# Optimization experiments

Measured on AMD Instinct MI355X. Metric: run time of the kernel, lower is better.

The kernel has to match this reference:

```python
import jax, jax.numpy as jnp
import numpy as np
import math

B, NO, ML, D, H = 32, 512, 512, 1024, 16


def setup_inputs() -> dict:
    key = jax.random.key(0)
    ks = jax.random.split(key, 16)
    v = jax.random.normal(ks[0], (B, NO, D), jnp.float32)
    t = jax.random.normal(ks[1], (B, ML, D), jnp.float32)
    # valid-length prefix masks (float, as in the torch module)
    v_len = jax.random.randint(ks[2], (B,), NO // 2, NO + 1)
    t_len = jax.random.randint(ks[3], (B,), ML // 2, ML + 1)
    v_mask = (jnp.arange(NO)[None, :] < v_len[:, None]).astype(jnp.float32)
    t_mask = (jnp.arange(ML)[None, :] < t_len[:, None]).astype(jnp.float32)
    lin = lambda k, din, dout: jax.random.normal(k, (din, dout), jnp.float32) * 0.02
    return {
        "v": v, "t": t, "v_mask": v_mask, "t_mask": t_mask,
        "W_v4t": lin(ks[4], D, D), "b_v4t": jnp.zeros((D,), jnp.float32),
        "W_t4v": lin(ks[5], D, D), "b_t4v": jnp.zeros((D,), jnp.float32),
        "W_v": lin(ks[6], D, 3 * D), "b_v": jnp.zeros((3 * D,), jnp.float32),
        "W_t": lin(ks[7], D, 3 * D), "b_t": jnp.zeros((3 * D,), jnp.float32),
        "W_vo": lin(ks[8], D, D), "b_vo": jnp.zeros((D,), jnp.float32),
        "W_to": lin(ks[9], D, D), "b_to": jnp.zeros((D,), jnp.float32),
        "num_head": H,
    }


def _heads(x, h, dh):
    b, n, _ = x.shape
    return x.reshape(b, n, h, dh).transpose(0, 2, 1, 3)  # [B,H,N,dh]


def _unheads(x):
    b, h, n, dh = x.shape
    return x.transpose(0, 2, 1, 3).reshape(b, n, h * dh)


def _attend(q, k, val, mask, gate, h, dh):
    # gate: [B, D] -> per-head diag scale [B,H,1,dh]
    g = 1.0 + gate.reshape(-1, h, 1, dh)
    scores = jnp.einsum('bhqd,bhkd->bhqk', g * q, g * k) / math.sqrt(dh)
    scores = jnp.where(mask[:, None, None, :] > 0, scores, -jnp.inf)
    attn = jax.nn.softmax(scores, axis=-1)
    return _unheads(jnp.einsum('bhqk,bhkd->bhqd', attn, val))


def reference(v, t, v_mask, t_mask, W_v4t, b_v4t, W_t4v, b_t4v,
              W_v, b_v, W_t, b_t, W_vo, b_vo, W_to, b_to, num_head):
    d = v.shape[-1]
    dh = d // num_head
    # masked mean pooling per modality
    v_mean = (v * v_mask[:, :, None]).sum(1) / v_mask.sum(1, keepdims=True)
    t_mean = (t * t_mask[:, :, None]).sum(1) / t_mask.sum(1, keepdims=True)
    v4t_gate = jax.nn.sigmoid(jax.nn.relu(v_mean) @ W_v4t + b_v4t)  # [B,D]
    t4v_gate = jax.nn.sigmoid(jax.nn.relu(t_mean) @ W_t4v + b_t4v)
    # fused KQV projections, masked
    v_trans = (jax.nn.relu(v) @ W_v + b_v) * v_mask[:, :, None]
    t_trans = (jax.nn.relu(t) @ W_t + b_t) * t_mask[:, :, None]
    # torch split order: k, q, v
    v_k, v_q, v_v = (_heads(v_trans[..., i * d:(i + 1) * d], num_head, dh) for i in range(3))
    t_k, t_q, t_v = (_heads(t_trans[..., i * d:(i + 1) * d], num_head, dh) for i in range(3))
    v_update = _attend(v_q, v_k, v_v, v_mask, t4v_gate, num_head, dh)
    t_update = _attend(t_q, t_k, t_v, t_mask, v4t_gate, num_head, dh)
    updated_v = (v + v_update) @ W_vo + b_vo
    updated_t = (t + t_update) @ W_to + b_to
    return updated_v, updated_t
```

## Files before the change

### kernel.cpp

```cpp
#include <hip/hip_runtime.h>
#include <hip/hip_bf16.h>
#include <math.h>

#define B_   32
#define NO_  512
#define D_   1024
#define H_   16
#define DH_  64
#define D3_  3072

typedef __hip_bfloat16 bf16;
typedef short short8  __attribute__((ext_vector_type(8)));
typedef short short4v __attribute__((ext_vector_type(4)));
typedef float f32x4   __attribute__((ext_vector_type(4)));

__device__ inline short f2bf(float x) {
  bf16 h = __float2bfloat16(x);
  return *reinterpret_cast<short*>(&h);
}
__device__ inline float bf2f(short s) {
  union { unsigned int u; float f; } cv;
  cv.u = ((unsigned int)(unsigned short)s) << 16;
  return cv.f;
}

__device__ inline void gload_lds16(const void* g, void* l) {
  __builtin_amdgcn_global_load_lds(
      (__attribute__((address_space(1))) void*)(void*)(g),
      (__attribute__((address_space(3))) void*)(l), 16, 0, 0);
}

__global__ __launch_bounds__(256) void pool_kernel(
    const float* __restrict__ v, const float* __restrict__ t,
    const float* __restrict__ vmask, const float* __restrict__ tmask,
    float* __restrict__ vmean, float* __restrict__ tmean) {
  const float* x; const float* m; float* out;
  if (blockIdx.y == 0) { x = v; m = vmask; out = vmean; }
  else                 { x = t; m = tmask; out = tmean; }
  int b = blockIdx.x >> 2;
  int d = ((blockIdx.x & 3) << 8) + threadIdx.x;
  float acc = 0.f, msum = 0.f;
  const float* xp = x + ((size_t)b * NO_) * D_ + d;
  const float* mp = m + b * NO_;
  for (int n = 0; n < NO_; ++n) {
    float mv = mp[n];
    acc  += xp[(size_t)n * D_] * mv;
    msum += mv;
  }
  out[b * D_ + d] = acc / msum;
}

__global__ __launch_bounds__(256) void gate_kernel(
    const float* __restrict__ vmean, const float* __restrict__ tmean,
    const float* __restrict__ Wv4t, const float* __restrict__ bv4t,
    const float* __restrict__ Wt4v, const float* __restrict__ bt4v,
    float* __restrict__ gv4t, float* __restrict__ gt4v) {
  const float* mean; const float* W; const float* bias; float* out;
  if (blockIdx.y == 0) { mean = vmean; W = Wv4t; bias = bv4t; out = gv4t; }
  else                 { mean = tmean; W = Wt4v; bias = bt4v; out = gt4v; }
  int b = blockIdx.x >> 2;
  int j = ((blockIdx.x & 3) << 8) + threadIdx.x;
  const float* mb = mean + b * D_;
  float acc = bias[j];
  for (int k = 0; k < D_; ++k) {
    float mv = mb[k]; mv = mv > 0.f ? mv : 0.f;
    acc += mv * W[(size_t)k * D_ + j];
  }
  out[b * D_ + j] = 1.f / (1.f + expf(-acc));
}

__global__ __launch_bounds__(256) void wtrans_kernel(
    const float* __restrict__ W, short* __restrict__ Wt, int K, int N) {
  __shared__ float tile[32][33];
  int n0 = blockIdx.x * 32, k0 = blockIdx.y * 32;
  int tx = threadIdx.x & 31, ty = threadIdx.x >> 5;
#pragma unroll
  for (int i = 0; i < 4; ++i) {
    int kk = ty + i * 8;
    tile[kk][tx] = W[(size_t)(k0 + kk) * N + n0 + tx];
  }
  __syncthreads();
#pragma unroll
  for (int i = 0; i < 4; ++i) {
    int nn = ty + i * 8;
    Wt[(size_t)(n0 + nn) * K + k0 + tx] = f2bf(tile[tx][nn]);
  }
}

__global__ __launch_bounds__(256) void reluconv_kernel(
    const float* __restrict__ x, short* __restrict__ y) {
  int i = (blockIdx.x * 256 + threadIdx.x) * 4;
  float4 vv = *(const float4*)(x + i);
  short4v o;
  o[0] = f2bf(vv.x > 0.f ? vv.x : 0.f);
  o[1] = f2bf(vv.y > 0.f ? vv.y : 0.f);
  o[2] = f2bf(vv.z > 0.f ? vv.z : 0.f);
  o[3] = f2bf(vv.w > 0.f ? vv.w : 0.f);
  *(short4v*)(y + i) = o;
}

__device__ __forceinline__ void stage_half(const short* __restrict__ g,
                                           short* l, int wave, int lane) {
#pragma unroll
  for (int r2 = 0; r2 < 2; ++r2) {
    int ob  = r2 * 8192 + wave * 1024;
    int o   = ob + lane * 16;
    int row = o >> 7;
    int kb  = (o & 127) ^ ((row & 7) << 4);
    gload_lds16(g + (size_t)row * D_ + (kb >> 1), l + (ob >> 1));
  }
}

__device__ __forceinline__ void read_a4(short8 (&a)[4][2], const short* As,
                                        int baseRow, int col, int qb) {
#pragma unroll
  for (int m = 0; m < 4; ++m) {
    int row = baseRow + m * 16 + col;
    int sw  = (row & 7) << 4;
    a[m][0] = *(const short8*)(As + (((row << 7) + (qb ^ sw)) >> 1));
    a[m][1] = *(const short8*)(As + (((row << 7) + ((64 + qb) ^ sw)) >> 1));
  }
}

__device__ __forceinline__ void read_b2(short8 (&b)[2][2], const short* Bs,
                                        int baseRow, int col, int qb) {
#pragma unroll
  for (int n = 0; n < 2; ++n) {
    int row = baseRow + n * 16 + col;
    int sw  = (row & 7) << 4;
    b[n][0] = *(const short8*)(Bs + (((row << 7) + (qb ^ sw)) >> 1));
    b[n][1] = *(const short8*)(Bs + (((row << 7) + ((64 + qb) ^ sw)) >> 1));
  }
}

template<int MH, int NH>
__device__ __forceinline__ void mma8(f32x4 (&acc)[8][4],
                                     const short8 (&a)[4][2],
                                     const short8 (&b)[2][2]) {
#pragma unroll
  for (int m = 0; m < 4; ++m)
#pragma unroll
    for (int n = 0; n < 2; ++n)
#pragma unroll
      for (int kh = 0; kh < 2; ++kh)
        acc[MH * 4 + m][NH * 2 + n] = __builtin_amdgcn_mfma_f32_16x16x32_bf16(
            a[m][kh], b[n][kh], acc[MH * 4 + m][NH * 2 + n], 0, 0, 0);
}

#define PHASE_TAIL(MH, NH, BR)                              \
  __builtin_amdgcn_s_barrier();                             \
  asm volatile("s_waitcnt lgkmcnt(0)" ::: "memory");        \
  __builtin_amdgcn_s_setprio(1);                            \
  mma8<MH, NH>(acc, a, BR);                                 \
  __builtin_amdgcn_s_setprio(0);                            \
  __builtin_amdgcn_s_barrier();

template<int SA, int SB, int VMN>
__device__ __forceinline__ void ktile(
    f32x4 (&acc)[8][4], short8 (&a)[4][2], short8 (&b0)[2][2], short8 (&b1)[2][2],
    const short* Asc, const short* Bsc, short* Asn, short* Bsn,
    const short* gA, const short* gB,
    int wm, int wn, int col, int qb, int wave, int lane) {
  read_a4(a, Asc, wm * 128, col, qb);
  read_b2(b0, Bsc, wn * 64, col, qb);
  if constexpr (SA) stage_half(gA, Asn, wave, lane);
  PHASE_TAIL(0, 0, b0)
  read_b2(b1, Bsc, wn * 64 + 32, col, qb);
  if constexpr (SA) stage_half(gA + 128 * D_, Asn + 8192, wave, lane);
  PHASE_TAIL(0, 1, b1)
  read_a4(a, Asc, wm * 128 + 64, col, qb);
  if constexpr (SB) stage_half(gB, Bsn, wave, lane);
  PHASE_TAIL(1, 0, b0)
  if constexpr (SB) stage_half(gB + 128 * D_, Bsn + 8192, wave, lane);
  __builtin_amdgcn_s_barrier();
  __builtin_amdgcn_s_setprio(1);
  mma8<1, 1>(acc, a, b1);
  __builtin_amdgcn_s_setprio(0);
  if constexpr (VMN >= 0)
    asm volatile("s_waitcnt vmcnt(%0)" :: "i"(VMN) : "memory");
  __builtin_amdgcn_s_barrier();
}

template<int EPI>
__global__ __launch_bounds__(512, 2) void mfma_gemm256_kernel(
    const short* __restrict__ A, const short* __restrict__ Bt,
    const float* __restrict__ bias, const float* __restrict__ mask,
    void* __restrict__ Cout, int M, int N) {
  __shared__ short lds[65536];
  short* As0 = lds;
  short* Bs0 = lds + 16384;
  short* As1 = lds + 32768;
  short* Bs1 = lds + 49152;

  const int tid  = threadIdx.x;
  const int wave = tid >> 6, lane = tid & 63;
  const int col  = lane & 15, quad = lane >> 4, qb = quad << 4;
  const int wm   = wave >> 2, wn = wave & 3;

  const int nx   = gridDim.x;
  const int orig = blockIdx.y * nx + blockIdx.x;
  const int cpx  = (nx * gridDim.y) >> 3;
  const int swz  = (orig & 7) * cpx + (orig >> 3);
  const int bx   = swz % nx;
  const int by   = swz / nx;
  const int rowBase = by * 256;
  const int colBase = bx * 256;

  const short* gA = A  + (size_t)rowBase * D_;
  const short* gB = Bt + (size_t)colBase * D_;

  f32x4 zero = {0.f, 0.f, 0.f, 0.f};
  f32x4 acc[8][4];
#pragma unroll
  for (int i = 0; i < 8; ++i)
#pragma unroll
    for (int j = 0; j < 4; ++j) acc[i][j] = zero;

  short8 a[4][2], b0[2][2], b1[2][2];

  stage_half(gA,                 As0,        wave, lane);
  stage_half(gA + 128 * D_,      As0 + 8192, wave, lane);
  stage_half(gB,                 Bs0,        wave, lane);
  stage_half(gB + 128 * D_,      Bs0 + 8192, wave, lane);
  stage_half(gB + 64,            Bs1,        wave, lane);
  stage_half(gB + 64 + 128 * D_, Bs1 + 8192, wave, lane);
  asm volatile("s_waitcnt vmcnt(4)" ::: "memory");
  __builtin_amdgcn_s_barrier();

  const short* gAk = gA + 64;
  const short* gBk = gB + 128;
  for (int i = 0; i < 7; ++i) {
    ktile<1, 1, 4>(acc, a, b0, b1, As0, Bs0, As1, Bs0, gAk,      gBk,
                   wm, wn, col, qb, wave, lane);
    ktile<1, 1, 4>(acc, a, b0, b1, As1, Bs1, As0, Bs1, gAk + 64, gBk + 64,
                   wm, wn, col, qb, wave, lane);
    gAk += 128; gBk += 128;
  }
  ktile<1, 0, 0>(acc, a, b0, b1, As0, Bs0, As1, Bs0, gAk, gBk,
                 wm, wn, col, qb, wave, lane);
  ktile<0, 0, -1>(acc, a, b0, b1, As1, Bs1, As0, Bs1, gAk, gBk,
                  wm, wn, col, qb, wave, lane);

#pragma unroll
  for (int mi = 0; mi < 8; ++mi) {
    const int row = rowBase + wm * 128 + mi * 16 + quad * 4;
    float mk[4];
    if (EPI == 0) {
#pragma unroll
      for (int r = 0; r < 4; ++r) mk[r] = mask[row + r];
    }
#pragma unroll
    for (int ni = 0; ni < 4; ++ni) {
      const int c = colBase + wn * 64 + ni * 16 + col;
      const float bv = bias[c];
#pragma unroll
      for (int r = 0; r < 4; ++r) {
        float val = acc[mi][ni][r] + bv;
        if (EPI == 0) {
          val *= mk[r];
          ((short*)Cout)[(size_t)(row + r) * N + c] = f2bf(val);
        } else {
          ((float*)Cout)[(size_t)(row + r) * N + c] = val;
        }
      }
    }
  }
}
#undef PHASE_TAIL

#define ATT_PAD 72

__global__ __launch_bounds__(256) void attn_mfma_kernel(
    const short* __restrict__ trans, const float* __restrict__ mask,
    const float* __restrict__ gate, const float* __restrict__ x,
    short* __restrict__ a2) {
  __shared__ short Ks[64 * ATT_PAD];
  __shared__ short Vt[64 * ATT_PAD];
  __shared__ short Ps[4][16 * ATT_PAD];
  __shared__ float lensh[4];

  const int tid  = threadIdx.x;
  const int wave = tid >> 6;
  const int lane = tid & 63;
  const int col  = lane & 15;
  const int quad = lane >> 4;
  const int b = blockIdx.z, h = blockIdx.y;
  const int qBase = blockIdx.x * 64 + wave * 16;

  const short* transB = trans + (size_t)b * NO_ * D3_;

  {
    float s = mask[b * NO_ + tid] + mask[b * NO_ + 256 + tid];
#pragma unroll
    for (int off = 1; off < 64; off <<= 1) s += __shfl_xor(s, off, 64);
    if (lane == 0) lensh[wave] = s;
  }

  short8 qf[2];
  {
    const int q = qBase + col;
    const short* qp = transB + (size_t)q * D3_ + D_ + h * DH_;
    const float* gp = gate + b * D_ + h * DH_;
#pragma unroll
    for (int f = 0; f < 2; ++f) {
      const int dh0 = f * 32 + quad * 8;
      short8 raw = *(const short8*)(qp + dh0);
      short8 sc;
#pragma unroll
      for (int j = 0; j < 8; ++j) {
        float g = 1.f + gp[dh0 + j];
        sc[j] = f2bf(bf2f(raw[j]) * g * g * 0.125f);
      }
      qf[f] = sc;
    }
  }
  __syncthreads();
  const int len = (int)(lensh[0] + lensh[1] + lensh[2] + lensh[3] + 0.5f);
  const int nch = (len + 63) >> 6;

  f32x4 O[4] = {{0,0,0,0},{0,0,0,0},{0,0,0,0},{0,0,0,0}};
  float m_i = -1e30f;
  float l_i = 0.f;

  const int key0 = tid >> 3;
  const int mseg = tid & 7;

  for (int ch = 0; ch < nch; ++ch) {
    __syncthreads();
#pragma unroll
    for (int half = 0; half < 2; ++half) {
      const int key = key0 + half * 32;
      const short* src = transB + (size_t)(ch * 64 + key) * D3_ + h * DH_ + mseg * 8;
      *(short8*)&Ks[key * ATT_PAD + mseg * 8] = *(const short8*)src;
      short8 vv = *(const short8*)(src + 2 * D_);
#pragma unroll
      for (int i = 0; i < 8; ++i) {
        int j = (i + mseg) & 7;
        Vt[(mseg * 8 + j) * ATT_PAD + key] = vv[j];
      }
    }
    __syncthreads();

    f32x4 St[4];
#pragma unroll
    for (int f = 0; f < 4; ++f) {
      const int krow = (f * 16 + col) * ATT_PAD;
      short8 kb0 = *(short8*)&Ks[krow + quad * 8];
      short8 kb1 = *(short8*)&Ks[krow + 32 + quad * 8];
      f32x4 acc = {0.f, 0.f, 0.f, 0.f};
      acc = __builtin_amdgcn_mfma_f32_16x16x32_bf16(kb0, qf[0], acc, 0, 0, 0);
      acc = __builtin_amdgcn_mfma_f32_16x16x32_bf16(kb1, qf[1], acc, 0, 0, 0);
      St[f] = acc;
    }

    const int kb0i = ch * 64 + quad * 4;
    float mloc = -1e30f;
    if (ch * 64 + 64 <= len) {
#pragma unroll
      for (int f = 0; f < 4; ++f)
#pragma unroll
        for (int r = 0; r < 4; ++r) mloc = fmaxf(mloc, St[f][r]);
    } else {
#pragma unroll
      for (int f = 0; f < 4; ++f)
#pragma unroll
        for (int r = 0; r < 4; ++r) {
          float s = (kb0i + f * 16 + r < len) ? St[f][r] : -1e30f;
          St[f][r] = s;
          mloc = fmaxf(mloc, s);
        }
    }
    mloc = fmaxf(mloc, __shfl_xor(mloc, 16, 64));
    mloc = fmaxf(mloc, __shfl_xor(mloc, 32, 64));
    const float mnew  = fmaxf(m_i, mloc);
    const float alpha = __expf(m_i - mnew);

    float psum = 0.f;
#pragma unroll
    for (int f = 0; f < 4; ++f) {
      float p0 = __expf(St[f][0] - mnew);
      float p1 = __expf(St[f][1] - mnew);
      float p2 = __expf(St[f][2] - mnew);
      float p3 = __expf(St[f][3] - mnew);
      psum += (p0 + p1) + (p2 + p3);
      unsigned u0 = (unsigned)(unsigned short)f2bf(p0) |
                    ((unsigned)(unsigned short)f2bf(p1) << 16);
      unsigned u1 = (unsigned)(unsigned short)f2bf(p2) |
                    ((unsigned)(unsigned short)f2bf(p3) << 16);
      const int base = col * ATT_PAD + f * 16 + quad * 4;
      *(unsigned*)&Ps[wave][base]     = u0;
      *(unsigned*)&Ps[wave][base + 2] = u1;
    }
    psum += __shfl_xor(psum, 16, 64);
    psum += __shfl_xor(psum, 32, 64);
    l_i = l_i * alpha + psum;
    m_i = mnew;

#pragma unroll
    for (int r = 0; r < 4; ++r) {
      float ar = __shfl(alpha, (quad << 4) + quad * 4 + r, 64);
#pragma unroll
      for (int t = 0; t < 4; ++t) O[t][r] *= ar;
    }

#pragma unroll
    for (int k2 = 0; k2 < 2; ++k2) {
      short8 pa = *(short8*)&Ps[wave][col * ATT_PAD + k2 * 32 + quad * 8];
#pragma unroll
      for (int t = 0; t < 4; ++t) {
        short8 vb = *(short8*)&Vt[(t * 16 + col) * ATT_PAD + k2 * 32 + quad * 8];
        O[t] = __builtin_amdgcn_mfma_f32_16x16x32_bf16(pa, vb, O[t], 0, 0, 0);
      }
    }
  }

  float lrec[4];
#pragma unroll
  for (int r = 0; r < 4; ++r)
    lrec[r] = 1.f / __shfl(l_i, (quad << 4) + quad * 4 + r, 64);
#pragma unroll
  for (int t = 0; t < 4; ++t) {
#pragma unroll
    for (int r = 0; r < 4; ++r) {
      int q = qBase + quad * 4 + r;
      size_t idx = ((size_t)b * NO_ + q) * D_ + h * DH_ + t * 16 + col;
      a2[idx] = f2bf(x[idx] + O[t][r] * lrec[r]);
    }
  }
}

extern "C" void kernel_launch(void* const* d_in, const int* in_sizes, int n_in,
                              void* d_out, int out_size, void* d_ws, size_t ws_size,
                              hipStream_t stream) {
  const float* v      = (const float*)d_in[0];
  const float* t      = (const float*)d_in[1];
  const float* v_mask = (const float*)d_in[2];
  const float* t_mask = (const float*)d_in[3];
  const float* W_v4t  = (const float*)d_in[4];
  const float* b_v4t  = (const float*)d_in[5];
  const float* W_t4v  = (const float*)d_in[6];
  const float* b_t4v  = (const float*)d_in[7];
  const float* W_v    = (const float*)d_in[8];
  const float* b_v    = (const float*)d_in[9];
  const float* W_t    = (const float*)d_in[10];
  const float* b_t    = (const float*)d_in[11];
  const float* W_vo   = (const float*)d_in[12];
  const float* b_vo   = (const float*)d_in[13];
  const float* W_to   = (const float*)d_in[14];
  const float* b_to   = (const float*)d_in[15];
  float* out = (float*)d_out;

  const size_t M = (size_t)B_ * NO_;

  float* ws     = (float*)d_ws;
  float* v_mean = ws;
  float* t_mean = v_mean + B_ * D_;
  float* g_v4t  = t_mean + B_ * D_;
  float* g_t4v  = g_v4t + B_ * D_;
  short* trans  = (short*)(g_t4v + B_ * D_);
  short* Abf    = trans + M * D3_;
  short* Wt_v   = Abf + M * D_;
  short* Wt_t   = Wt_v + (size_t)D3_ * D_;
  short* Wt_vo  = Wt_t + (size_t)D3_ * D_;
  short* Wt_to  = Wt_vo + (size_t)D_ * D_;

  pool_kernel<<<dim3(B_ * 4, 2), 256, 0, stream>>>(v, t, v_mask, t_mask, v_mean, t_mean);
  gate_kernel<<<dim3(B_ * 4, 2), 256, 0, stream>>>(v_mean, t_mean, W_v4t, b_v4t,
                                                   W_t4v, b_t4v, g_v4t, g_t4v);

  wtrans_kernel<<<dim3(D3_ / 32, D_ / 32), 256, 0, stream>>>(W_v,  Wt_v,  D_, D3_);
  wtrans_kernel<<<dim3(D3_ / 32, D_ / 32), 256, 0, stream>>>(W_t,  Wt_t,  D_, D3_);
  wtrans_kernel<<<dim3(D_ / 32,  D_ / 32), 256, 0, stream>>>(W_vo, Wt_vo, D_, D_);
  wtrans_kernel<<<dim3(D_ / 32,  D_ / 32), 256, 0, stream>>>(W_to, Wt_to, D_, D_);

  dim3 kqv_grid(D3_ / 256, M / 256);
  dim3 out_grid(D_ / 256,  M / 256);
  dim3 att_grid(NO_ / 64, H_, B_);
  int  conv_blocks = (int)(M * D_ / (256 * 4));

  reluconv_kernel<<<conv_blocks, 256, 0, stream>>>(v, Abf);
  mfma_gemm256_kernel<0><<<kqv_grid, 512, 0, stream>>>(Abf, Wt_v, b_v, v_mask,
                                                       trans, (int)M, D3_);
  attn_mfma_kernel<<<att_grid, 256, 0, stream>>>(trans, v_mask, g_t4v, v, Abf);
  mfma_gemm256_kernel<1><<<out_grid, 512, 0, stream>>>(Abf, Wt_vo, b_vo, nullptr,
                                                       out, (int)M, D_);

  reluconv_kernel<<<conv_blocks, 256, 0, stream>>>(t, Abf);
  mfma_gemm256_kernel<0><<<kqv_grid, 512, 0, stream>>>(Abf, Wt_t, b_t, t_mask,
                                                       trans, (int)M, D3_);
  attn_mfma_kernel<<<att_grid, 256, 0, stream>>>(trans, t_mask, g_v4t, t, Abf);
  mfma_gemm256_kernel<1><<<out_grid, 512, 0, stream>>>(Abf, Wt_to, b_to, nullptr,
                                                       out + M * D_, (int)M, D_);
}
```

Before: 824.8 us.

## Double the attention key tile and prefetch next K/V chunk into registers

The attention kernel now processes 128 keys per iteration instead of 64 and loads the next K/V chunk from global memory into registers before computing on the current chunk. The registers are written to shared memory only after the PV matmul, so global load latency overlaps with MFMA and softmax work, and there are half as many barrier pairs. In exchange it uses more registers and shared memory, which may lower occupancy. Padding and masking waste at the tail also grows for lengths that are not multiples of 128.

```diff
diff --git a/kernel.cpp b/kernel.cpp
--- a/kernel.cpp
+++ b/kernel.cpp
@@ -268,15 +268,17 @@
 }
 #undef PHASE_TAIL
 
-#define ATT_PAD 72
+#define KVB   128
+#define KPAD  72
+#define VPAD  136
 
 __global__ __launch_bounds__(256) void attn_mfma_kernel(
     const short* __restrict__ trans, const float* __restrict__ mask,
     const float* __restrict__ gate, const float* __restrict__ x,
     short* __restrict__ a2) {
-  __shared__ short Ks[64 * ATT_PAD];
-  __shared__ short Vt[64 * ATT_PAD];
-  __shared__ short Ps[4][16 * ATT_PAD];
+  __shared__ short Ks[KVB * KPAD];
+  __shared__ short Vt[64 * VPAD];
+  __shared__ short Ps[4][16 * VPAD];
   __shared__ float lensh[4];
 
   const int tid  = threadIdx.x;
@@ -316,7 +318,7 @@
   }
   __syncthreads();
   const int len = (int)(lensh[0] + lensh[1] + lensh[2] + lensh[3] + 0.5f);
-  const int nch = (len + 63) >> 6;
+  const int nch = (len + KVB - 1) >> 7;
 
   f32x4 O[4] = {{0,0,0,0},{0,0,0,0},{0,0,0,0},{0,0,0,0}};
   float m_i = -1e30f;
@@ -325,26 +327,42 @@
   const int key0 = tid >> 3;
   const int mseg = tid & 7;
 
+  short8 kreg[4], vreg[4];
+
+#pragma unroll
+  for (int half = 0; half < 4; ++half) {
+    const short* src = transB + (size_t)(key0 + half * 32) * D3_ + h * DH_ + mseg * 8;
+    kreg[half] = *(const short8*)src;
+    vreg[half] = *(const short8*)(src + 2 * D_);
+  }
+#pragma unroll
+  for (int half = 0; half < 4; ++half) {
+    const int key = key0 + half * 32;
+    *(short8*)&Ks[key * KPAD + mseg * 8] = kreg[half];
+#pragma unroll
+    for (int i = 0; i < 8; ++i) {
+      int j = (i + mseg) & 7;
+      Vt[(mseg * 8 + j) * VPAD + key] = vreg[half][j];
+    }
+  }
+  __syncthreads();
+
   for (int ch = 0; ch < nch; ++ch) {
-    __syncthreads();
-#pragma unroll
-    for (int half = 0; half < 2; ++half) {
-      const int key = key0 + half * 32;
-      const short* src = transB + (size_t)(ch * 64 + key) * D3_ + h * DH_ + mseg * 8;
-      *(short8*)&Ks[key * ATT_PAD + mseg * 8] = *(const short8*)src;
-      short8 vv = *(const short8*)(src + 2 * D_);
-#pragma unroll
-      for (int i = 0; i < 8; ++i) {
-        int j = (i + mseg) & 7;
-        Vt[(mseg * 8 + j) * ATT_PAD + key] = vv[j];
+    const bool more = (ch + 1 < nch);
+    if (more) {
+#pragma unroll
+      for (int half = 0; half < 4; ++half) {
+        const short* src = transB +
+            (size_t)((ch + 1) * KVB + key0 + half * 32) * D3_ + h * DH_ + mseg * 8;
+        kreg[half] = *(const short8*)src;
+        vreg[half] = *(const short8*)(src + 2 * D_);
       }
     }
-    __syncthreads();
-
-    f32x4 St[4];
-#pragma unroll
-    for (int f = 0; f < 4; ++f) {
-      const int krow = (f * 16 + col) * ATT_PAD;
+
+    f32x4 St[8];
+#pragma unroll
+    for (int f = 0; f < 8; ++f) {
+      const int krow = (f * 16 + col) * KPAD;
       short8 kb0 = *(short8*)&Ks[krow + quad * 8];
       short8 kb1 = *(short8*)&Ks[krow + 32 + quad * 8];
       f32x4 acc = {0.f, 0.f, 0.f, 0.f};
@@ -353,16 +371,16 @@
       St[f] = acc;
     }
 
-    const int kb0i = ch * 64 + quad * 4;
+    const int kb0i = ch * KVB + quad * 4;
     float mloc = -1e30f;
-    if (ch * 64 + 64 <= len) {
-#pragma unroll
-      for (int f = 0; f < 4; ++f)
+    if (ch * KVB + KVB <= len) {
+#pragma unroll
+      for (int f = 0; f < 8; ++f)
 #pragma unroll
         for (int r = 0; r < 4; ++r) mloc = fmaxf(mloc, St[f][r]);
     } else {
 #pragma unroll
-      for (int f = 0; f < 4; ++f)
+      for (int f = 0; f < 8; ++f)
 #pragma unroll
         for (int r = 0; r < 4; ++r) {
           float s = (kb0i + f * 16 + r < len) ? St[f][r] : -1e30f;
@@ -377,7 +395,7 @@
 
     float psum = 0.f;
 #pragma unroll
-    for (int f = 0; f < 4; ++f) {
+    for (int f = 0; f < 8; ++f) {
       float p0 = __expf(St[f][0] - mnew);
       float p1 = __expf(St[f][1] - mnew);
       float p2 = __expf(St[f][2] - mnew);
@@ -387,7 +405,7 @@
                     ((unsigned)(unsigned short)f2bf(p1) << 16);
       unsigned u1 = (unsigned)(unsigned short)f2bf(p2) |
                     ((unsigned)(unsigned short)f2bf(p3) << 16);
-      const int base = col * ATT_PAD + f * 16 + quad * 4;
+      const int base = col * VPAD + f * 16 + quad * 4;
       *(unsigned*)&Ps[wave][base]     = u0;
       *(unsigned*)&Ps[wave][base + 2] = u1;
     }
@@ -404,13 +422,28 @@
     }
 
 #pragma unroll
-    for (int k2 = 0; k2 < 2; ++k2) {
-      short8 pa = *(short8*)&Ps[wave][col * ATT_PAD + k2 * 32 + quad * 8];
+    for (int k2 = 0; k2 < 4; ++k2) {
+      short8 pa = *(short8*)&Ps[wave][col * VPAD + k2 * 32 + quad * 8];
 #pragma unroll
       for (int t = 0; t < 4; ++t) {
-        short8 vb = *(short8*)&Vt[(t * 16 + col) * ATT_PAD + k2 * 32 + quad * 8];
+        short8 vb = *(short8*)&Vt[(t * 16 + col) * VPAD + k2 * 32 + quad * 8];
         O[t] = __builtin_amdgcn_mfma_f32_16x16x32_bf16(pa, vb, O[t], 0, 0, 0);
       }
+    }
+
+    if (more) {
+      __syncthreads();
+#pragma unroll
+      for (int half = 0; half < 4; ++half) {
+        const int key = key0 + half * 32;
+        *(short8*)&Ks[key * KPAD + mseg * 8] = kreg[half];
+#pragma unroll
+        for (int i = 0; i < 8; ++i) {
+          int j = (i + mseg) & 7;
+          Vt[(mseg * 8 + j) * VPAD + key] = vreg[half][j];
+        }
+      }
+      __syncthreads();
     }
   }
 
```

Result: slower. 871.6 us (+5.7%).

## Prefetch next K/V chunk into registers and XOR-swizzle transposed V in LDS

Applied to the files above, without the earlier changes.

The attention loop now issues the global loads for the next 64-key K/V chunk into registers before computing on the current chunk, then writes them to shared memory after the PV MFMAs. This is meant to hide global load latency behind compute. The transposed V tile is also stored with an XOR swizzle on the key column, and the read index is adjusted to match, to reduce LDS bank conflicts. In exchange the kernel uses more registers, which may lower occupancy.

```diff
diff --git a/kernel.cpp b/kernel.cpp
--- a/kernel.cpp
+++ b/kernel.cpp
@@ -325,21 +325,36 @@
   const int key0 = tid >> 3;
   const int mseg = tid & 7;
 
+  short8 kreg[2], vreg[2];
+
+#pragma unroll
+  for (int half = 0; half < 2; ++half) {
+    const short* src = transB + (size_t)(key0 + half * 32) * D3_ + h * DH_ + mseg * 8;
+    kreg[half] = *(const short8*)src;
+    vreg[half] = *(const short8*)(src + 2 * D_);
+  }
+#pragma unroll
+  for (int half = 0; half < 2; ++half) {
+    const int key  = key0 + half * 32;
+    *(short8*)&Ks[key * ATT_PAD + mseg * 8] = kreg[half];
+    const int kcol = key ^ (mseg << 3);
+#pragma unroll
+    for (int i = 0; i < 8; ++i)
+      Vt[(mseg * 8 + i) * ATT_PAD + kcol] = vreg[half][i];
+  }
+  __syncthreads();
+
   for (int ch = 0; ch < nch; ++ch) {
-    __syncthreads();
-#pragma unroll
-    for (int half = 0; half < 2; ++half) {
-      const int key = key0 + half * 32;
-      const short* src = transB + (size_t)(ch * 64 + key) * D3_ + h * DH_ + mseg * 8;
-      *(short8*)&Ks[key * ATT_PAD + mseg * 8] = *(const short8*)src;
-      short8 vv = *(const short8*)(src + 2 * D_);
-#pragma unroll
-      for (int i = 0; i < 8; ++i) {
-        int j = (i + mseg) & 7;
-        Vt[(mseg * 8 + j) * ATT_PAD + key] = vv[j];
+    const bool more = (ch + 1 < nch);
+    if (more) {
+#pragma unroll
+      for (int half = 0; half < 2; ++half) {
+        const short* src = transB +
+            (size_t)((ch + 1) * 64 + key0 + half * 32) * D3_ + h * DH_ + mseg * 8;
+        kreg[half] = *(const short8*)src;
+        vreg[half] = *(const short8*)(src + 2 * D_);
       }
     }
-    __syncthreads();
 
     f32x4 St[4];
 #pragma unroll
@@ -408,9 +423,25 @@
       short8 pa = *(short8*)&Ps[wave][col * ATT_PAD + k2 * 32 + quad * 8];
 #pragma unroll
       for (int t = 0; t < 4; ++t) {
-        short8 vb = *(short8*)&Vt[(t * 16 + col) * ATT_PAD + k2 * 32 + quad * 8];
+        const int r  = t * 16 + col;
+        const int ck = (k2 * 4 + quad) ^ ((2 * t + (col >> 3)) & 7);
+        short8 vb = *(short8*)&Vt[r * ATT_PAD + ck * 8];
         O[t] = __builtin_amdgcn_mfma_f32_16x16x32_bf16(pa, vb, O[t], 0, 0, 0);
       }
+    }
+
+    if (more) {
+      __syncthreads();
+#pragma unroll
+      for (int half = 0; half < 2; ++half) {
+        const int key  = key0 + half * 32;
+        *(short8*)&Ks[key * ATT_PAD + mseg * 8] = kreg[half];
+        const int kcol = key ^ (mseg << 3);
+#pragma unroll
+        for (int i = 0; i < 8; ++i)
+          Vt[(mseg * 8 + i) * ATT_PAD + kcol] = vreg[half][i];
+      }
+      __syncthreads();
     }
   }
 
```

Measured after the change: 819.7 us. No clear change (-0.6%).
